# Kernel tuning notes

Hardware: AMD Instinct MI355X
Metric: run time of the kernel (lower is better)

Reference implementation:

```python
import jax, jax.numpy as jnp
import numpy as np

K_NEIGHBORS = 1  # self.K + self.J = 1 + 0
FP_H = 56        # sqrt(args.fp_nums) = sqrt(3136)


def setup_inputs() -> dict:
    key = jax.random.key(0)
    k1, k2 = jax.random.split(key)
    embeds = jax.random.normal(k1, (32, 3136, 1024), dtype=jnp.float32)
    centroids = jax.random.normal(k2, (2048, 1024), dtype=jnp.float32)
    return {"embeds": embeds, "centroids": centroids}


def reference(embeds, centroids):
    # embeds: [B, N, D]; centroids: [M, D]
    B, N, D = embeds.shape
    # squared L2 distance via ||e||^2 + ||c||^2 - 2 e.c  (same expansion as torch code)
    feat_sq = jnp.sum(embeds * embeds, axis=2, keepdims=True)          # [B, N, 1]
    cent_sq = jnp.sum(centroids * centroids, axis=1)[None, None, :]    # [1, 1, M]
    cross = jnp.einsum('bnd,md->bnm', embeds, centroids)               # [B, N, M]
    d2 = feat_sq + cent_sq - 2.0 * cross
    # clamp tiny negative fp error before sqrt (torch sqrt would NaN there)
    dist = jnp.sqrt(jnp.maximum(d2, 0.0))                              # [B, N, M]
    # k smallest distances (ascending), k = K + J = 1
    neg_top, _ = jax.lax.top_k(-dist, K_NEIGHBORS)
    d_top = -neg_top                                                   # [B, N, k]
    # softmin over the k neighbors, weight the nearest distance
    sim = jax.nn.softmax(-d_top, axis=-1)[:, :, 0] * d_top[:, :, 0]    # [B, N]
    # rearrange 'b (h w) c -> b c h w' with c = 1
    score = sim.reshape(B, FP_H, FP_H)[:, None, :, :]                  # [B, 1, 56, 56]
    # eval mode: loss = 0; embeds is passed through unchanged, so return score
    return score
```

## Files before the change

### kernel.cpp

```cpp
#include <hip/hip_runtime.h>
#include <hip/hip_bf16.h>


typedef __bf16 bf16x8 __attribute__((ext_vector_type(8)));
typedef __bf16 bf16x4 __attribute__((ext_vector_type(4)));
typedef float f32x4 __attribute__((ext_vector_type(4)));
typedef int i32x4 __attribute__((ext_vector_type(4)));
typedef int i32x8 __attribute__((ext_vector_type(8)));

#define N_ROWS 100352
#define M_CENT 2048
#define D_K 1024

#define BM4 128
#define BN4 128
#define BK4 128
#define NT4 (D_K / BK4)
#define NCT4 (M_CENT / BN4)
#define NBLK4 ((N_ROWS / BM4) * NCT4)
#define BPX4 (NBLK4 / 8)

#define TM 128
#define TN 128
#define BK 64
#define NT_TILES (M_CENT / TN)
#define KT_STEPS (D_K / BK)

#define AS1 __attribute__((address_space(1)))
#define AS3 __attribute__((address_space(3)))

#define WAITVM(N) asm volatile("s_waitcnt vmcnt(" #N ")" ::: "memory")
#define LGKM0 asm volatile("s_waitcnt lgkmcnt(0)" ::: "memory")
#define FENCE asm volatile("" ::: "memory")

__global__ __launch_bounds__(256) void rowsq_fp8pack(const float* __restrict__ src,
                                                     unsigned char* __restrict__ dst,
                                                     float* __restrict__ sq) {
  const int m = blockIdx.x;
  const int t = threadIdx.x;
  const float4 v = *reinterpret_cast<const float4*>(src + (size_t)m * D_K + t * 4);
  int pk = __builtin_amdgcn_cvt_pk_fp8_f32(v.x, v.y, 0, false);
  pk = __builtin_amdgcn_cvt_pk_fp8_f32(v.z, v.w, pk, true);
  const int k = t * 4;
  const int seg = k >> 7;
  const int ksi = (k >> 5) & 3;
  const int g = (k >> 3) & 3;
  const int j = k & 7;
  const int p = seg * 128 + (((ksi >> 1) * 4 + g) << 4) + (ksi & 1) * 8 + j;
  *reinterpret_cast<unsigned int*>(dst + (size_t)m * D_K + p) = (unsigned int)pk;
  float ss = v.x * v.x + v.y * v.y + v.z * v.z + v.w * v.w;
  ss += __shfl_xor(ss, 1);
  ss += __shfl_xor(ss, 2);
  ss += __shfl_xor(ss, 4);
  ss += __shfl_xor(ss, 8);
  ss += __shfl_xor(ss, 16);
  ss += __shfl_xor(ss, 32);
  __shared__ float ws4[4];
  const int w = t >> 6, l = t & 63;
  if (l == 0) ws4[w] = ss;
  __syncthreads();
  if (t == 0) sq[m] = ws4[0] + ws4[1] + ws4[2] + ws4[3];
}

__global__ __launch_bounds__(256, 3) void gemm_min_mx(const unsigned char* __restrict__ e8,
                                                      const unsigned char* __restrict__ c8,
                                                      const float* __restrict__ csq,
                                                      float* __restrict__ pmin) {
  __shared__ __align__(16) char lds[32768];
  __shared__ float rowmin2[2][BM4];

  const int t = threadIdx.x;
  const int w = t >> 6;
  const int l = t & 63;
  const int wr = w >> 1, wc = w & 1;
  const int g = l >> 4, lr = l & 15;

  const int b = blockIdx.x;
  const int swz = (b & 7) * BPX4 + (b >> 3);
  const int rp = swz >> 4, ct = swz & 15;
  const long row0 = (long)rp * BM4;
  const int col0 = ct * BN4;

  const int trow = t >> 3, tsl = t & 7;
  const int ssw = (tsl ^ (trow & 7)) << 4;
  const unsigned char* srcA0 = e8 + (row0 + trow) * (size_t)D_K + ssw;
  const unsigned char* srcB0 = c8 + (size_t)(col0 + trow) * D_K + ssw;
  const int dst0 = t * 16;

  f32x4 acc[4][4];
#pragma unroll
  for (int m = 0; m < 4; ++m)
#pragma unroll
    for (int n = 0; n < 4; ++n) acc[m][n] = (f32x4){0.f, 0.f, 0.f, 0.f};

  const int swsel = lr & 7;
  const char* aBase0 = lds + (wr * 64 + lr) * 128 + ((g ^ swsel) << 4);
  const char* aBase1 = lds + (wr * 64 + lr) * 128 + (((4 + g) ^ swsel) << 4);
  const char* bBase0 = lds + 16384 + (wc * 64 + lr) * 128 + ((g ^ swsel) << 4);
  const char* bBase1 = lds + 16384 + (wc * 64 + lr) * 128 + (((4 + g) ^ swsel) << 4);

  auto stage = [&](int kt) {
    const size_t ko = (size_t)kt * BK4;
#pragma unroll
    for (int i = 0; i < 4; ++i)
      __builtin_amdgcn_global_load_lds(
          (const AS1 unsigned int*)(const void*)(srcA0 + (size_t)i * 32 * D_K + ko),
          (AS3 unsigned int*)(void*)(lds + i * 4096 + dst0), 16, 0, 0);
#pragma unroll
    for (int i = 0; i < 4; ++i)
      __builtin_amdgcn_global_load_lds(
          (const AS1 unsigned int*)(const void*)(srcB0 + (size_t)i * 32 * D_K + ko),
          (AS3 unsigned int*)(void*)(lds + 16384 + i * 4096 + dst0), 16, 0, 0);
  };

  auto compute_tile = [&]() {
    i32x8 b8[4];
#pragma unroll
    for (int n = 0; n < 4; ++n) {
      const i32x4 lo = *reinterpret_cast<const i32x4*>(bBase0 + n * 2048);
      const i32x4 hi = *reinterpret_cast<const i32x4*>(bBase1 + n * 2048);
      b8[n] = __builtin_shufflevector(lo, hi, 0, 1, 2, 3, 4, 5, 6, 7);
    }
#pragma unroll
    for (int m = 0; m < 4; ++m) {
      const i32x4 lo = *reinterpret_cast<const i32x4*>(aBase0 + m * 2048);
      const i32x4 hi = *reinterpret_cast<const i32x4*>(aBase1 + m * 2048);
      const i32x8 a8 = __builtin_shufflevector(lo, hi, 0, 1, 2, 3, 4, 5, 6, 7);
#pragma unroll
      for (int n = 0; n < 4; ++n)
        acc[m][n] = __builtin_amdgcn_mfma_scale_f32_16x16x128_f8f6f4(
            a8, b8[n], acc[m][n], 0 , 0 , 0, 0x7F7F7F7F, 0,
            0x7F7F7F7F);
    }
  };

  stage(0);
#pragma unroll
  for (int kt = 0; kt < NT4; ++kt) {
    WAITVM(0);
    FENCE;
    __builtin_amdgcn_s_barrier();
    FENCE;
    compute_tile();
    if (kt < NT4 - 1) {
      LGKM0;
      FENCE;
      __builtin_amdgcn_s_barrier();
      FENCE;
      stage(kt + 1);
    }
  }

  float runmin[4][4];
#pragma unroll
  for (int m = 0; m < 4; ++m)
#pragma unroll
    for (int r = 0; r < 4; ++r) runmin[m][r] = 3.0e38f;
#pragma unroll
  for (int n = 0; n < 4; ++n) {
    const float cs = csq[col0 + wc * 64 + n * 16 + lr];
#pragma unroll
    for (int m = 0; m < 4; ++m)
#pragma unroll
      for (int r = 0; r < 4; ++r)
        runmin[m][r] = fminf(runmin[m][r], cs - 2.0f * acc[m][n][r]);
  }
#pragma unroll
  for (int m = 0; m < 4; ++m)
#pragma unroll
    for (int r = 0; r < 4; ++r) {
      float v = runmin[m][r];
      v = fminf(v, __shfl_xor(v, 1));
      v = fminf(v, __shfl_xor(v, 2));
      v = fminf(v, __shfl_xor(v, 4));
      v = fminf(v, __shfl_xor(v, 8));
      runmin[m][r] = v;
    }
  if (lr == 0) {
#pragma unroll
    for (int m = 0; m < 4; ++m)
#pragma unroll
      for (int r = 0; r < 4; ++r)
        rowmin2[wc][wr * 64 + m * 16 + g * 4 + r] = runmin[m][r];
  }
  __syncthreads();
  if (t < BM4) {
    pmin[(row0 + t) * NCT4 + ct] = fminf(rowmin2[0][t], rowmin2[1][t]);
  }
}

__global__ __launch_bounds__(256) void final_min(const float* __restrict__ esq,
                                                 const float* __restrict__ pmin,
                                                 float* __restrict__ out) {
  const int r = blockIdx.x * 256 + threadIdx.x;
  const float4* p = reinterpret_cast<const float4*>(pmin + (size_t)r * 16);
  float4 a = p[0], b = p[1], c = p[2], d = p[3];
  float m = fminf(fminf(fminf(a.x, a.y), fminf(a.z, a.w)),
                  fminf(fminf(b.x, b.y), fminf(b.z, b.w)));
  m = fminf(m, fminf(fminf(fminf(c.x, c.y), fminf(c.z, c.w)),
                     fminf(fminf(d.x, d.y), fminf(d.z, d.w))));
  out[r] = sqrtf(fmaxf(esq[r] + m, 0.f));
}

__global__ __launch_bounds__(256) void rowsq_bf16(const float* __restrict__ src,
                                                  __bf16* __restrict__ dst,
                                                  float* __restrict__ sq) {
  const int m = blockIdx.x;
  const int t = threadIdx.x;
  const float4 v = *reinterpret_cast<const float4*>(src + (size_t)m * D_K + t * 4);
  bf16x4 o = {(__bf16)v.x, (__bf16)v.y, (__bf16)v.z, (__bf16)v.w};
  *reinterpret_cast<bf16x4*>(dst + (size_t)m * D_K + t * 4) = o;
  float ss = v.x * v.x + v.y * v.y + v.z * v.z + v.w * v.w;
  ss += __shfl_xor(ss, 1);
  ss += __shfl_xor(ss, 2);
  ss += __shfl_xor(ss, 4);
  ss += __shfl_xor(ss, 8);
  ss += __shfl_xor(ss, 16);
  ss += __shfl_xor(ss, 32);
  __shared__ float ws4[4];
  const int w = t >> 6, l = t & 63;
  if (l == 0) ws4[w] = ss;
  __syncthreads();
  if (t == 0) sq[m] = ws4[0] + ws4[1] + ws4[2] + ws4[3];
}

template <bool WS>
__global__ __launch_bounds__(256, 2) void fused_min(const float* __restrict__ embeds,
                                                    const float* __restrict__ centf,
                                                    const __bf16* __restrict__ cbf,
                                                    const float* __restrict__ csq,
                                                    float* __restrict__ out) {
  __shared__ __align__(16) char Ab[TM * 128];
  __shared__ __align__(16) char Bb[TN * 128];
  __shared__ float rowmin2[2][TM];
  __shared__ float sqrow[TM];
  __shared__ float colsq[TN];

  const int t = threadIdx.x;
  const int w = t >> 6;
  const int l = t & 63;
  const int wr = w >> 1, wc = w & 1;
  const int g = l >> 4, lr = l & 15;
  const long row0 = (long)blockIdx.x * TM;

  float runmin[4][4];
#pragma unroll
  for (int m = 0; m < 4; ++m)
#pragma unroll
    for (int r = 0; r < 4; ++r) runmin[m][r] = 3.0e38f;

  float sqpart[8];
#pragma unroll
  for (int c = 0; c < 8; ++c) sqpart[c] = 0.f;

  for (int nt = 0; nt < NT_TILES; ++nt) {
    const int col0 = nt * TN;
    f32x4 acc[4][4];
#pragma unroll
    for (int m = 0; m < 4; ++m)
#pragma unroll
      for (int n = 0; n < 4; ++n) acc[m][n] = (f32x4){0.f, 0.f, 0.f, 0.f};

    float cpart[8];
    if constexpr (!WS) {
#pragma unroll
      for (int c = 0; c < 8; ++c) cpart[c] = 0.f;
    }

    for (int kt = 0; kt < KT_STEPS; ++kt) {
      __syncthreads();
      if constexpr (WS) {
#pragma unroll
        for (int i = 0; i < 4; ++i) {
          const int s = (w * 4 + i) * 64 + l;
          const int col = s >> 3, sl = s & 7;
          const __bf16* src =
              cbf + (size_t)(col0 + col) * D_K + kt * BK + ((sl ^ (col & 7)) << 3);
          __builtin_amdgcn_global_load_lds(
              (const AS1 unsigned int*)(const void*)src,
              (AS3 unsigned int*)(void*)(Bb + (w * 4 + i) * 1024), 16, 0, 0);
        }
      } else {
#pragma unroll
        for (int c = 0; c < 8; ++c) {
          const int f = c * 256 + t;
          const int col = f >> 4, kq = f & 15;
          const float4 v = *reinterpret_cast<const float4*>(
              centf + (size_t)(col0 + col) * D_K + kt * BK + kq * 4);
          cpart[c] += v.x * v.x + v.y * v.y + v.z * v.z + v.w * v.w;
          bf16x4 o = {(__bf16)v.x, (__bf16)v.y, (__bf16)v.z, (__bf16)v.w};
          const int slot = kq >> 1;
          *reinterpret_cast<bf16x4*>(Bb + col * 128 + ((slot ^ (col & 7)) << 4) +
                                     (kq & 1) * 8) = o;
        }
      }
#pragma unroll
      for (int c = 0; c < 8; ++c) {
        const int f = c * 256 + t;
        const int row = f >> 4, kq = f & 15;
        const float4 v = *reinterpret_cast<const float4*>(
            embeds + (row0 + row) * (long)D_K + kt * BK + kq * 4);
        if (nt == 0) sqpart[c] += v.x * v.x + v.y * v.y + v.z * v.z + v.w * v.w;
        bf16x4 o = {(__bf16)v.x, (__bf16)v.y, (__bf16)v.z, (__bf16)v.w};
        const int slot = kq >> 1;
        *reinterpret_cast<bf16x4*>(Ab + row * 128 + ((slot ^ (row & 7)) << 4) +
                                   (kq & 1) * 8) = o;
      }
      __syncthreads();
#pragma unroll
      for (int ks = 0; ks < 2; ++ks) {
        bf16x8 af[4], bfr[4];
#pragma unroll
        for (int m = 0; m < 4; ++m) {
          const int row = wr * 64 + m * 16 + lr;
          const int slot = ks * 4 + g;
          af[m] = *reinterpret_cast<const bf16x8*>(Ab + row * 128 +
                                                   ((slot ^ (row & 7)) << 4));
        }
#pragma unroll
        for (int n = 0; n < 4; ++n) {
          const int col = wc * 64 + n * 16 + lr;
          const int slot = ks * 4 + g;
          bfr[n] = *reinterpret_cast<const bf16x8*>(Bb + col * 128 +
                                                    ((slot ^ (col & 7)) << 4));
        }
#pragma unroll
        for (int m = 0; m < 4; ++m)
#pragma unroll
          for (int n = 0; n < 4; ++n)
            acc[m][n] =
                __builtin_amdgcn_mfma_f32_16x16x32_bf16(af[m], bfr[n], acc[m][n], 0, 0, 0);
      }
    }

    if (nt == 0) {
#pragma unroll
      for (int c = 0; c < 8; ++c) {
        float ss = sqpart[c];
        ss += __shfl_xor(ss, 1);
        ss += __shfl_xor(ss, 2);
        ss += __shfl_xor(ss, 4);
        ss += __shfl_xor(ss, 8);
        if (lr == 0) sqrow[c * 16 + (w * 4 + g)] = ss;
      }
    }
    if constexpr (!WS) {
#pragma unroll
      for (int c = 0; c < 8; ++c) {
        float ss = cpart[c];
        ss += __shfl_xor(ss, 1);
        ss += __shfl_xor(ss, 2);
        ss += __shfl_xor(ss, 4);
        ss += __shfl_xor(ss, 8);
        if (lr == 0) colsq[c * 16 + (w * 4 + g)] = ss;
      }
      __syncthreads();
    }

#pragma unroll
    for (int n = 0; n < 4; ++n) {
      float cs;
      if constexpr (WS)
        cs = csq[col0 + wc * 64 + n * 16 + lr];
      else
        cs = colsq[wc * 64 + n * 16 + lr];
#pragma unroll
      for (int m = 0; m < 4; ++m)
#pragma unroll
        for (int r = 0; r < 4; ++r)
          runmin[m][r] = fminf(runmin[m][r], cs - 2.0f * acc[m][n][r]);
    }
  }

#pragma unroll
  for (int m = 0; m < 4; ++m)
#pragma unroll
    for (int r = 0; r < 4; ++r) {
      float v = runmin[m][r];
      v = fminf(v, __shfl_xor(v, 1));
      v = fminf(v, __shfl_xor(v, 2));
      v = fminf(v, __shfl_xor(v, 4));
      v = fminf(v, __shfl_xor(v, 8));
      runmin[m][r] = v;
    }
  if (lr == 0) {
#pragma unroll
    for (int m = 0; m < 4; ++m)
#pragma unroll
      for (int r = 0; r < 4; ++r)
        rowmin2[wc][wr * 64 + m * 16 + g * 4 + r] = runmin[m][r];
  }
  __syncthreads();
  if (t < TM) {
    const float v = fminf(rowmin2[0][t], rowmin2[1][t]);
    out[row0 + t] = sqrtf(fmaxf(sqrow[t] + v, 0.f));
  }
}

extern "C" void kernel_launch(void* const* d_in, const int* in_sizes, int n_in,
                              void* d_out, int out_size, void* d_ws, size_t ws_size,
                              hipStream_t stream) {
  const float* embeds = (const float*)d_in[0];
  const float* cent = (const float*)d_in[1];
  float* out = (float*)d_out;

  const size_t off_c8 = 0;
  const size_t off_csq = off_c8 + (size_t)M_CENT * D_K;
  const size_t off_e8 = off_csq + (size_t)M_CENT * 4;
  const size_t off_esq = off_e8 + (size_t)N_ROWS * D_K;
  const size_t off_pmin = off_esq + (size_t)N_ROWS * 4;
  const size_t need_full = off_pmin + (size_t)N_ROWS * NCT4 * 4;
  const size_t need_small = (size_t)M_CENT * D_K * 2 + (size_t)M_CENT * 4;

  if (ws_size >= need_full) {
    unsigned char* c8 = (unsigned char*)d_ws + off_c8;
    float* csq = (float*)((char*)d_ws + off_csq);
    unsigned char* e8 = (unsigned char*)d_ws + off_e8;
    float* esq = (float*)((char*)d_ws + off_esq);
    float* pmin = (float*)((char*)d_ws + off_pmin);
    rowsq_fp8pack<<<M_CENT, 256, 0, stream>>>(cent, c8, csq);
    rowsq_fp8pack<<<N_ROWS, 256, 0, stream>>>(embeds, e8, esq);
    gemm_min_mx<<<NBLK4, 256, 0, stream>>>(e8, c8, csq, pmin);
    final_min<<<N_ROWS / 256, 256, 0, stream>>>(esq, pmin, out);
  } else if (ws_size >= need_small) {
    __bf16* cbf = (__bf16*)d_ws;
    float* csq = (float*)((char*)d_ws + (size_t)M_CENT * D_K * 2);
    rowsq_bf16<<<M_CENT, 256, 0, stream>>>(cent, cbf, csq);
    fused_min<true><<<N_ROWS / TM, 256, 0, stream>>>(embeds, cent, cbf, csq, out);
  } else {
    fused_min<false><<<N_ROWS / TM, 256, 0, stream>>>(embeds, cent, nullptr, nullptr, out);
  }
}
```

Measured before the change: 320.4 us.

## Double-buffer LDS staging in fp8 GEMM-min kernel to overlap loads with MFMA

Doubles the LDS allocation to two 32KB buffers and prefetches the tile two k-steps ahead. The wait now allows 8 outstanding global-to-LDS loads, so the next tile's fetch can overlap the current tile's MFMA work instead of stalling on the full wait each step. In exchange, occupancy drops from 3 to 2 blocks per CU (launch bounds and the larger LDS footprint), which reduces latency hiding across blocks.

Measured after the change: 349.8 us. 9.2% more time.

```diff
diff --git a/kernel.cpp b/kernel.cpp
--- a/kernel.cpp
+++ b/kernel.cpp
@@ -19,6 +19,7 @@
 #define NCT4 (M_CENT / BN4)
 #define NBLK4 ((N_ROWS / BM4) * NCT4)
 #define BPX4 (NBLK4 / 8)
+#define BUFSZ4 32768
 
 #define TM 128
 #define TN 128
@@ -62,11 +63,11 @@
   if (t == 0) sq[m] = ws4[0] + ws4[1] + ws4[2] + ws4[3];
 }
 
-__global__ __launch_bounds__(256, 3) void gemm_min_mx(const unsigned char* __restrict__ e8,
+__global__ __launch_bounds__(256, 2) void gemm_min_mx(const unsigned char* __restrict__ e8,
                                                       const unsigned char* __restrict__ c8,
                                                       const float* __restrict__ csq,
                                                       float* __restrict__ pmin) {
-  __shared__ __align__(16) char lds[32768];
+  __shared__ __align__(16) char lds[2 * BUFSZ4];
   __shared__ float rowmin2[2][BM4];
 
   const int t = threadIdx.x;
@@ -99,32 +100,33 @@
   const char* bBase0 = lds + 16384 + (wc * 64 + lr) * 128 + ((g ^ swsel) << 4);
   const char* bBase1 = lds + 16384 + (wc * 64 + lr) * 128 + (((4 + g) ^ swsel) << 4);
 
-  auto stage = [&](int kt) {
+  auto stage = [&](int kt, int buf) {
     const size_t ko = (size_t)kt * BK4;
+    char* base = lds + buf * BUFSZ4;
 #pragma unroll
     for (int i = 0; i < 4; ++i)
       __builtin_amdgcn_global_load_lds(
           (const AS1 unsigned int*)(const void*)(srcA0 + (size_t)i * 32 * D_K + ko),
-          (AS3 unsigned int*)(void*)(lds + i * 4096 + dst0), 16, 0, 0);
+          (AS3 unsigned int*)(void*)(base + i * 4096 + dst0), 16, 0, 0);
 #pragma unroll
     for (int i = 0; i < 4; ++i)
       __builtin_amdgcn_global_load_lds(
           (const AS1 unsigned int*)(const void*)(srcB0 + (size_t)i * 32 * D_K + ko),
-          (AS3 unsigned int*)(void*)(lds + 16384 + i * 4096 + dst0), 16, 0, 0);
+          (AS3 unsigned int*)(void*)(base + 16384 + i * 4096 + dst0), 16, 0, 0);
   };
 
-  auto compute_tile = [&]() {
+  auto compute_tile = [&](int bo) {
     i32x8 b8[4];
 #pragma unroll
     for (int n = 0; n < 4; ++n) {
-      const i32x4 lo = *reinterpret_cast<const i32x4*>(bBase0 + n * 2048);
-      const i32x4 hi = *reinterpret_cast<const i32x4*>(bBase1 + n * 2048);
+      const i32x4 lo = *reinterpret_cast<const i32x4*>(bBase0 + bo + n * 2048);
+      const i32x4 hi = *reinterpret_cast<const i32x4*>(bBase1 + bo + n * 2048);
       b8[n] = __builtin_shufflevector(lo, hi, 0, 1, 2, 3, 4, 5, 6, 7);
     }
 #pragma unroll
     for (int m = 0; m < 4; ++m) {
-      const i32x4 lo = *reinterpret_cast<const i32x4*>(aBase0 + m * 2048);
-      const i32x4 hi = *reinterpret_cast<const i32x4*>(aBase1 + m * 2048);
+      const i32x4 lo = *reinterpret_cast<const i32x4*>(aBase0 + bo + m * 2048);
+      const i32x4 hi = *reinterpret_cast<const i32x4*>(aBase1 + bo + m * 2048);
       const i32x8 a8 = __builtin_shufflevector(lo, hi, 0, 1, 2, 3, 4, 5, 6, 7);
 #pragma unroll
       for (int n = 0; n < 4; ++n)
@@ -134,20 +136,26 @@
     }
   };
 
-  stage(0);
+  stage(0, 0);
+  stage(1, 1);
 #pragma unroll
   for (int kt = 0; kt < NT4; ++kt) {
-    WAITVM(0);
+    const int buf = kt & 1;
+    if (kt < NT4 - 1) {
+      WAITVM(8);
+    } else {
+      WAITVM(0);
+    }
     FENCE;
     __builtin_amdgcn_s_barrier();
     FENCE;
-    compute_tile();
-    if (kt < NT4 - 1) {
+    compute_tile(buf * BUFSZ4);
+    if (kt < NT4 - 2) {
       LGKM0;
       FENCE;
       __builtin_amdgcn_s_barrier();
       FENCE;
-      stage(kt + 1);
+      stage(kt + 2, buf);
     }
   }
 
```

## Load centroid fragments directly from global into registers, bypassing LDS

Applied to the files above, without the earlier changes.

The centroid (B) operand no longer goes through shared memory. Each wave now loads its own MFMA B fragments from global memory straight into registers, issued alongside the async A-tile copy into LDS. This halves the LDS footprint and removes the LDS reads for B. In exchange, B data is fetched redundantly by the two wave rows, register pressure rises, and B load latency is only hidden behind the A-tile wait.

Measured after the change: 494.5 us. +54.3%, slower.

```diff
diff --git a/kernel.cpp b/kernel.cpp
--- a/kernel.cpp
+++ b/kernel.cpp
@@ -66,7 +66,7 @@
                                                       const unsigned char* __restrict__ c8,
                                                       const float* __restrict__ csq,
                                                       float* __restrict__ pmin) {
-  __shared__ __align__(16) char lds[32768];
+  __shared__ __align__(16) char lds[16384];
   __shared__ float rowmin2[2][BM4];
 
   const int t = threadIdx.x;
@@ -84,8 +84,12 @@
   const int trow = t >> 3, tsl = t & 7;
   const int ssw = (tsl ^ (trow & 7)) << 4;
   const unsigned char* srcA0 = e8 + (row0 + trow) * (size_t)D_K + ssw;
-  const unsigned char* srcB0 = c8 + (size_t)(col0 + trow) * D_K + ssw;
   const int dst0 = t * 16;
+
+  const unsigned char* colB[4];
+#pragma unroll
+  for (int n = 0; n < 4; ++n)
+    colB[n] = c8 + (size_t)(col0 + wc * 64 + n * 16 + lr) * D_K + g * 16;
 
   f32x4 acc[4][4];
 #pragma unroll
@@ -96,31 +100,31 @@
   const int swsel = lr & 7;
   const char* aBase0 = lds + (wr * 64 + lr) * 128 + ((g ^ swsel) << 4);
   const char* aBase1 = lds + (wr * 64 + lr) * 128 + (((4 + g) ^ swsel) << 4);
-  const char* bBase0 = lds + 16384 + (wc * 64 + lr) * 128 + ((g ^ swsel) << 4);
-  const char* bBase1 = lds + 16384 + (wc * 64 + lr) * 128 + (((4 + g) ^ swsel) << 4);
-
-  auto stage = [&](int kt) {
+
+  i32x4 bLo[4], bHi[4];
+
+  auto stageA = [&](int kt) {
     const size_t ko = (size_t)kt * BK4;
 #pragma unroll
     for (int i = 0; i < 4; ++i)
       __builtin_amdgcn_global_load_lds(
           (const AS1 unsigned int*)(const void*)(srcA0 + (size_t)i * 32 * D_K + ko),
           (AS3 unsigned int*)(void*)(lds + i * 4096 + dst0), 16, 0, 0);
-#pragma unroll
-    for (int i = 0; i < 4; ++i)
-      __builtin_amdgcn_global_load_lds(
-          (const AS1 unsigned int*)(const void*)(srcB0 + (size_t)i * 32 * D_K + ko),
-          (AS3 unsigned int*)(void*)(lds + 16384 + i * 4096 + dst0), 16, 0, 0);
+  };
+
+  auto loadB = [&](int kt) {
+#pragma unroll
+    for (int n = 0; n < 4; ++n) {
+      bLo[n] = *reinterpret_cast<const i32x4*>(colB[n] + kt * 128);
+      bHi[n] = *reinterpret_cast<const i32x4*>(colB[n] + kt * 128 + 64);
+    }
   };
 
   auto compute_tile = [&]() {
     i32x8 b8[4];
 #pragma unroll
-    for (int n = 0; n < 4; ++n) {
-      const i32x4 lo = *reinterpret_cast<const i32x4*>(bBase0 + n * 2048);
-      const i32x4 hi = *reinterpret_cast<const i32x4*>(bBase1 + n * 2048);
-      b8[n] = __builtin_shufflevector(lo, hi, 0, 1, 2, 3, 4, 5, 6, 7);
-    }
+    for (int n = 0; n < 4; ++n)
+      b8[n] = __builtin_shufflevector(bLo[n], bHi[n], 0, 1, 2, 3, 4, 5, 6, 7);
 #pragma unroll
     for (int m = 0; m < 4; ++m) {
       const i32x4 lo = *reinterpret_cast<const i32x4*>(aBase0 + m * 2048);
@@ -134,10 +138,12 @@
     }
   };
 
-  stage(0);
+  stageA(0);
+  FENCE;
+  loadB(0);
 #pragma unroll
   for (int kt = 0; kt < NT4; ++kt) {
-    WAITVM(0);
+    WAITVM(8);
     FENCE;
     __builtin_amdgcn_s_barrier();
     FENCE;
@@ -147,7 +153,9 @@
       FENCE;
       __builtin_amdgcn_s_barrier();
       FENCE;
-      stage(kt + 1);
+      stageA(kt + 1);
+      FENCE;
+      loadB(kt + 1);
     }
   }
 
```
